# Kernel tuning notes

Hardware: AMD Instinct MI355X
Metric: run time of the kernel (lower is better)

## Reference

```python
import jax, jax.numpy as jnp
import numpy as np

D_SNP, D_MODEL, N_HEADS = 512, 512, 8
D_K = D_MODEL // N_HEADS
TEMPERATURE = 1.0
NEG = -1e9


def setup_inputs() -> dict:
    key = jax.random.key(0)
    ks = jax.random.split(key, 16)
    B, G, S = 4, 1024, 4096
    inp = {
        'queries': jax.random.normal(ks[0], (B, G, D_SNP), jnp.float32),
        'keys_values': jax.random.normal(ks[1], (B, S, D_SNP), jnp.float32),
        'dq': jax.random.normal(ks[2], (B, 1, D_MODEL), jnp.float32),
        'dk': jax.random.normal(ks[3], (B, 1, D_MODEL), jnp.float32),
        'mask': jax.random.randint(ks[4], (B, S), 0, 2, jnp.int32),
        'cis_mask': jax.random.randint(ks[5], (G, S), 0, 2, jnp.int32).astype(bool),
        'wq_w': jax.random.normal(ks[6], (D_MODEL, D_SNP), jnp.float32) * 0.02,
        'wq_b': jnp.zeros((D_MODEL,), jnp.float32),
        'wk_w': jax.random.normal(ks[7], (D_MODEL, D_SNP), jnp.float32) * 0.02,
        'wk_b': jnp.zeros((D_MODEL,), jnp.float32),
        'wv_w': jax.random.normal(ks[8], (D_MODEL, D_SNP), jnp.float32) * 0.02,
        'wv_b': jnp.zeros((D_MODEL,), jnp.float32),
        'wo_w': jax.random.normal(ks[9], (D_MODEL, D_MODEL), jnp.float32) * 0.02,
        'wo_b': jnp.zeros((D_MODEL,), jnp.float32),
        'ln_g': jnp.ones((D_MODEL,), jnp.float32),
        'ln_b': jnp.zeros((D_MODEL,), jnp.float32),
    }
    return inp


def _layer_norm(x, g, b, eps=1e-5):
    mu = jnp.mean(x, axis=-1, keepdims=True)
    var = jnp.var(x, axis=-1, keepdims=True)
    return (x - mu) * jax.lax.rsqrt(var + eps) * g + b


def reference(queries, keys_values, dq, dk, mask, cis_mask,
              wq_w, wq_b, wk_w, wk_b, wv_w, wv_b, wo_w, wo_b, ln_g, ln_b):
    B, G, _ = queries.shape
    S = keys_values.shape[1]
    # Linear projections (torch Linear: x @ W^T + b) + env shifts
    Q = queries @ wq_w.T + wq_b + dq          # [B, G, D]
    K = keys_values @ wk_w.T + wk_b + dk      # [B, S, D]
    V = keys_values @ wv_w.T + wv_b           # [B, S, D]
    # split heads: [B, H, len, d_k]
    Q = Q.reshape(B, G, N_HEADS, D_K).transpose(0, 2, 1, 3)
    K = K.reshape(B, S, N_HEADS, D_K).transpose(0, 2, 1, 3)
    V = V.reshape(B, S, N_HEADS, D_K).transpose(0, 2, 1, 3)
    scale = 1.0 / (TEMPERATURE * np.sqrt(D_K).astype(np.float32))
    scores = jnp.einsum('bhgd,bhsd->bhgs', Q, K) * scale  # [B,H,G,S]
    # cis structural mask: True = cis (kept)
    scores = jnp.where(cis_mask[None, None, :, :], scores, NEG)
    # padding mask: 1 = valid
    scores = jnp.where(mask[:, None, None, :] == 0, NEG, scores)
    attn = jax.nn.softmax(scores, axis=-1)    # dropout=0 in eval
    out = jnp.einsum('bhgs,bhsd->bhgd', attn, V)
    out = out.transpose(0, 2, 1, 3).reshape(B, G, D_MODEL)
    out = out @ wo_w.T + wo_b
    return _layer_norm(out, ln_g, ln_b)
```

## Files before the change

### kernel.cpp

```cpp
#include <hip/hip_runtime.h>
#include <stdint.h>
#include <stddef.h>

typedef __bf16 bf16;
typedef __bf16 bf16x4 __attribute__((ext_vector_type(4)));
typedef __bf16 bf16x8 __attribute__((ext_vector_type(8)));
typedef float f32x4 __attribute__((ext_vector_type(4)));
typedef float f32x16 __attribute__((ext_vector_type(16)));
typedef unsigned long long u64;

#define BATCH 4
#define G_LEN 1024
#define S_LEN 4096
#define DM 512
#define NH 8
#define DK 64
#define CIS_WORDS (G_LEN * (S_LEN / 64))
#define NQ_EL  (BATCH * G_LEN * DM)
#define NKV_EL (BATCH * S_LEN * DM)
#define NW_EL  (DM * DM)
#define PACK_BLOCKS ((CIS_WORDS + BATCH * (S_LEN / 64) + 3) / 4)
#define CVT_BLOCKS  ((NQ_EL + NKV_EL + 4 * NW_EL) / 2048)
#define QSCALE (0.125f * 1.44269504f)

__device__ __forceinline__ f32x4 mfma16(bf16x8 a, bf16x8 b, f32x4 c) {
    return __builtin_amdgcn_mfma_f32_16x16x32_bf16(a, b, c, 0, 0, 0);
}
__device__ __forceinline__ f32x16 mfma32(bf16x8 a, bf16x8 b, f32x16 c) {
    return __builtin_amdgcn_mfma_f32_32x32x16_bf16(a, b, c, 0, 0, 0);
}
__device__ __forceinline__ uint32_t cvtpk(float lo, float hi_) {
    uint32_t r;
    asm("v_cvt_pk_bf16_f32 %0, %1, %2" : "=v"(r) : "v"(lo), "v"(hi_));
    return r;
}
__device__ __forceinline__ void pswap(uint32_t& a, uint32_t& b) {
    asm("v_permlane32_swap_b32 %0, %1" : "+v"(a), "+v"(b));
}
__device__ __forceinline__ float fexp2(float x) {
    float r;
    asm("v_exp_f32 %0, %1" : "=v"(r) : "v"(x));
    return r;
}
__device__ __forceinline__ bf16x8 mk8(uint32_t a, uint32_t b, uint32_t c, uint32_t d) {
    union { uint32_t u[4]; bf16x8 v; } x;
    x.u[0] = a; x.u[1] = b; x.u[2] = c; x.u[3] = d;
    return x.v;
}
__device__ __forceinline__ void exppack(f32x16& c, uint32_t kw, float& lsum,
                                        bf16x8& pa0, bf16x8& pa1) {
    #pragma unroll
    for (int reg = 0; reg < 16; ++reg) {
        const int bit = (reg & 3) + 8 * (reg >> 2);
        const float e = fexp2(c[reg]);
        c[reg] = ((kw >> bit) & 1u) ? e : 0.f;
    }
    lsum += ((c[0] + c[1]) + (c[2] + c[3])) + ((c[4] + c[5]) + (c[6] + c[7]))
          + ((c[8] + c[9]) + (c[10] + c[11])) + ((c[12] + c[13]) + (c[14] + c[15]));
    uint32_t wa0 = cvtpk(c[0],  c[1]),  wa1 = cvtpk(c[2],  c[3]);
    uint32_t wb0 = cvtpk(c[4],  c[5]),  wb1 = cvtpk(c[6],  c[7]);
    uint32_t wc0 = cvtpk(c[8],  c[9]),  wc1 = cvtpk(c[10], c[11]);
    uint32_t wd0 = cvtpk(c[12], c[13]), wd1 = cvtpk(c[14], c[15]);
    pswap(wa0, wb0); pswap(wa1, wb1); pswap(wc0, wd0); pswap(wc1, wd1);
    pa0 = mk8(wa0, wa1, wb0, wb1);
    pa1 = mk8(wc0, wc1, wd0, wd1);
}
__device__ __forceinline__ void stage16(const bf16* g, char* l) {
    __builtin_amdgcn_global_load_lds(
        (const __attribute__((address_space(1))) void*)g,
        (__attribute__((address_space(3))) void*)l, 16, 0, 0);
}

__global__ __launch_bounds__(256) void prep(
    const void* __restrict__ cisv, const int* __restrict__ mask,
    const float* __restrict__ q, const float* __restrict__ kv,
    const float* __restrict__ wq, const float* __restrict__ wk,
    const float* __restrict__ wv, const float* __restrict__ wo,
    u64* __restrict__ cbits, u64* __restrict__ mbits,
    bf16* __restrict__ oq, bf16* __restrict__ okv, bf16* __restrict__ ow4)
{
    const int bid = blockIdx.x;
    if (bid < PACK_BLOCKS) {
        const unsigned char* cis8 = (const unsigned char*)cisv;
        const int lane = threadIdx.x & 63;
        const int is_byte = __any((int)cis8[4 * lane + 1]);
        const int wid = bid * 4 + (threadIdx.x >> 6);
        if (wid < CIS_WORDS) {
            int v;
            if (is_byte) v = cis8[(size_t)wid * 64 + lane];
            else         v = ((const int*)cisv)[(size_t)wid * 64 + lane];
            const u64 bits = __ballot(v != 0);
            if (lane == 0) cbits[wid] = bits;
        } else if (wid < CIS_WORDS + BATCH * (S_LEN / 64)) {
            const int w2 = wid - CIS_WORDS;
            const u64 bits = __ballot(mask[w2 * 64 + lane] != 0);
            if (lane == 0) mbits[w2] = bits;
        }
        return;
    }
    const size_t e = ((size_t)(bid - PACK_BLOCKS) * 256 + threadIdx.x) * 8;
    const float* src;
    bf16* dst;
    size_t off;
    if (e < NQ_EL)               { src = q;  dst = oq;  off = e; }
    else if (e < NQ_EL + NKV_EL) { src = kv; dst = okv; off = e - NQ_EL; }
    else {
        const size_t w = e - NQ_EL - NKV_EL;
        const int wi = (int)(w / NW_EL);
        off = w % NW_EL;
        src = (wi == 0) ? wq : (wi == 1) ? wk : (wi == 2) ? wv : wo;
        dst = ow4 + (size_t)wi * NW_EL;
    }
    const float4 a = *(const float4*)(src + off);
    const float4 b = *(const float4*)(src + off + 4);
    bf16x8 o;
    o[0] = (bf16)a.x; o[1] = (bf16)a.y; o[2] = (bf16)a.z; o[3] = (bf16)a.w;
    o[4] = (bf16)b.x; o[5] = (bf16)b.y; o[6] = (bf16)b.z; o[7] = (bf16)b.w;
    *(bf16x8*)(dst + off) = o;
}

template<int OUT_F32, int ROWS_PER_B>
__global__ __launch_bounds__(256) void gemm64(
    const bf16* __restrict__ A, const bf16* __restrict__ B,
    const float* __restrict__ bias, const float* __restrict__ shift,
    void* __restrict__ Out, float oscale)
{
    __shared__ bf16 As[64][72];
    __shared__ bf16 Bs[64][72];
    const int tid  = threadIdx.x;
    const int lane = tid & 63;
    const int wave = tid >> 6;
    const int l15  = lane & 15;
    const int l4   = lane >> 4;
    const int m0   = blockIdx.x * 64;
    const int n0   = blockIdx.y * 64;

    f32x4 acc[4] = {};

    for (int kt = 0; kt < DM; kt += 64) {
        #pragma unroll
        for (int i = 0; i < 2; ++i) {
            const int q   = tid + i * 256;
            const int row = q >> 3;
            const int kq  = (q & 7) * 8;
            *(bf16x8*)&As[row][kq] = *(const bf16x8*)(A + (size_t)(m0 + row) * DM + kt + kq);
            *(bf16x8*)&Bs[row][kq] = *(const bf16x8*)(B + (size_t)(n0 + row) * DM + kt + kq);
        }
        __syncthreads();
        #pragma unroll
        for (int ks = 0; ks < 64; ks += 32) {
            const bf16x8 a = *(const bf16x8*)&As[wave * 16 + l15][ks + 8 * l4];
            #pragma unroll
            for (int n = 0; n < 4; ++n) {
                const bf16x8 b = *(const bf16x8*)&Bs[n * 16 + l15][ks + 8 * l4];
                acc[n] = mfma16(a, b, acc[n]);
            }
        }
        __syncthreads();
    }

    #pragma unroll
    for (int n = 0; n < 4; ++n) {
        const int col = n0 + n * 16 + l15;
        const float bv = bias[col];
        #pragma unroll
        for (int r = 0; r < 4; ++r) {
            const int m = m0 + wave * 16 + l4 * 4 + r;
            float v = acc[n][r] + bv;
            if (shift) v += shift[(m / ROWS_PER_B) * DM + col];
            v *= oscale;
            if (OUT_F32) ((float*)Out)[(size_t)m * DM + col] = v;
            else         ((bf16*)Out)[(size_t)m * DM + col] = (bf16)v;
        }
    }
}

__global__ __launch_bounds__(256) void gemm_kvq128(
    const bf16* __restrict__ Xkv, const bf16* __restrict__ Xq,
    const bf16* __restrict__ Wk, const float* __restrict__ bk, const float* __restrict__ dkv,
    const bf16* __restrict__ Wv, const float* __restrict__ bv,
    const bf16* __restrict__ Wq, const float* __restrict__ bq, const float* __restrict__ dq,
    bf16* __restrict__ OutK, bf16* __restrict__ OutVt, bf16* __restrict__ OutQ)
{
    const int z = blockIdx.z;
    if (z == 2 && blockIdx.x >= 32) return;

    __shared__ bf16 As[128][72];
    __shared__ bf16 Bs[128][72];
    const int tid  = threadIdx.x;
    const int lane = tid & 63;
    const int wave = tid >> 6;
    const int l15  = lane & 15;
    const int l4   = lane >> 4;
    const int wr   = wave >> 1;
    const int wc   = wave & 1;
    const int m0   = blockIdx.x * 128;
    const int n0   = blockIdx.y * 128;
    const bf16* X = (z == 2) ? Xq : Xkv;
    const bf16* W = (z == 0) ? Wk : (z == 1) ? Wv : Wq;

    f32x4 acc[4][4] = {};

    for (int kt = 0; kt < DM; kt += 64) {
        #pragma unroll
        for (int i = 0; i < 4; ++i) {
            const int q   = tid + i * 256;
            const int row = q >> 3;
            const int kq  = (q & 7) * 8;
            *(bf16x8*)&As[row][kq] = *(const bf16x8*)(X + (size_t)(m0 + row) * DM + kt + kq);
            *(bf16x8*)&Bs[row][kq] = *(const bf16x8*)(W + (size_t)(n0 + row) * DM + kt + kq);
        }
        __syncthreads();
        #pragma unroll
        for (int ks = 0; ks < 64; ks += 32) {
            bf16x8 af[4];
            #pragma unroll
            for (int mi = 0; mi < 4; ++mi)
                af[mi] = *(const bf16x8*)&As[wr * 64 + mi * 16 + l15][ks + 8 * l4];
            #pragma unroll
            for (int n = 0; n < 4; ++n) {
                const bf16x8 b = *(const bf16x8*)&Bs[wc * 64 + n * 16 + l15][ks + 8 * l4];
                #pragma unroll
                for (int mi = 0; mi < 4; ++mi)
                    acc[mi][n] = mfma16(af[mi], b, acc[mi][n]);
            }
        }
        __syncthreads();
    }

    #pragma unroll
    for (int n = 0; n < 4; ++n) {
        const int col = n0 + wc * 64 + n * 16 + l15;
        #pragma unroll
        for (int mi = 0; mi < 4; ++mi) {
            const int mb = m0 + wr * 64 + mi * 16 + l4 * 4;
            if (z == 1) {
                const int bb = mb >> 12;
                const float bvc = bv[col];
                bf16x4 o;
                #pragma unroll
                for (int r = 0; r < 4; ++r) o[r] = (bf16)(acc[mi][n][r] + bvc);
                *(bf16x4*)(OutVt + ((size_t)bb * DM + col) * 4096 + (mb & 4095)) = o;
            } else if (z == 0) {
                const int bb = mb >> 12;
                const float s = bk[col] + dkv[bb * DM + col];
                #pragma unroll
                for (int r = 0; r < 4; ++r)
                    OutK[(size_t)(mb + r) * DM + col] = (bf16)(acc[mi][n][r] + s);
            } else {
                const int bb = mb >> 10;
                const float s = bq[col] + dq[bb * DM + col];
                #pragma unroll
                for (int r = 0; r < 4; ++r)
                    OutQ[(size_t)(mb + r) * DM + col] = (bf16)((acc[mi][n][r] + s) * QSCALE);
            }
        }
    }
}

__global__ __launch_bounds__(256) void attn_kernel(
    const bf16* __restrict__ Qb, const bf16* __restrict__ Kb,
    const bf16* __restrict__ Vt, const u64* __restrict__ mbits,
    const u64* __restrict__ cbits, bf16* __restrict__ PO, float* __restrict__ PL)
{
    __shared__ __align__(16) char sm[32768];

    const int tid  = threadIdx.x;
    const int lane = tid & 63;
    const int wave = tid >> 6;
    const int l31  = lane & 31;
    const int hi   = lane >> 5;

    const int flat = blockIdx.x;
    const int xcd  = flat & 7;
    const int slot = flat >> 3;
    const int pr   = xcd * 4 + (slot >> 5);
    const int sub  = slot & 31;
    const int b    = pr >> 3;
    const int h    = pr & 7;
    const int g0   = (sub >> 2) * 128;
    const int tb   = (sub & 3) * 16;
    const int blkid = pr * 32 + sub;

    const bf16* qbase = Qb + (size_t)(b * G_LEN + g0 + wave * 32 + l31) * DM + h * DK + 8 * hi;
    const bf16x8 qf0 = *(const bf16x8*)(qbase);
    const bf16x8 qf1 = *(const bf16x8*)(qbase + 16);
    const bf16x8 qf2 = *(const bf16x8*)(qbase + 32);
    const bf16x8 qf3 = *(const bf16x8*)(qbase + 48);

    const bf16* Kh = Kb + (size_t)b * S_LEN * DM + h * DK;
    const bf16* Vh = Vt + (size_t)(b * NH + h) * DK * S_LEN;
    const u64*  mbv = mbits + b * (S_LEN / 64);
    const u64*  cbv = cbits + (size_t)(g0 + wave * 32 + l31) * (S_LEN / 64);

    const bool isK    = (wave < 2);
    const int rowbase = (wave & 1) * 32 + (lane >> 3);
    const int col16s  = (lane & 7) ^ (rowbase & 7);
    const int swz     = l31 & 7;

#define STAGE(tt, bufi) do {                                                   \
    char* ldw = sm + (bufi) * 16384 + wave * 4096;                             \
    _Pragma("unroll")                                                          \
    for (int i = 0; i < 4; ++i) {                                              \
        const int row = rowbase + i * 8;                                       \
        const bf16* g = isK                                                    \
            ? (Kh + (size_t)((tt) * 64 + row) * DM + col16s * 8)               \
            : (Vh + (size_t)row * S_LEN + (tt) * 64 + col16s * 8);             \
        stage16(g, ldw + i * 1024);                                            \
    }                                                                          \
} while (0)

    f32x16 accA = {};
    f32x16 accB = {};
    float lsum = 0.f;

    STAGE(tb + 0, 0);

    for (int t = 0; t < 16; ++t) {
        __builtin_amdgcn_s_barrier();
        __builtin_amdgcn_sched_barrier(0);
        if (t + 1 < 16) {
            STAGE(tb + t + 1, (t + 1) & 1);
            asm volatile("s_waitcnt vmcnt(4)" ::: "memory");
        } else {
            asm volatile("s_waitcnt vmcnt(0)" ::: "memory");
        }
        __builtin_amdgcn_s_barrier();
        __builtin_amdgcn_sched_barrier(0);

        const char* bK = sm + (t & 1) * 16384;
        const char* bV = bK + 8192;

#define KF(ss, m) (*(const bf16x8*)(bK + ((ss) * 32 + l31) * 128 + (((2 * (m) + hi) ^ swz) * 16)))
        f32x16 c0 = {}, c1 = {};
        __builtin_amdgcn_s_setprio(1);
        c0 = mfma32(KF(0, 0), qf0, c0); c0 = mfma32(KF(0, 1), qf1, c0);
        c0 = mfma32(KF(0, 2), qf2, c0); c0 = mfma32(KF(0, 3), qf3, c0);
        c1 = mfma32(KF(1, 0), qf0, c1); c1 = mfma32(KF(1, 1), qf1, c1);
        c1 = mfma32(KF(1, 2), qf2, c1); c1 = mfma32(KF(1, 3), qf3, c1);
        __builtin_amdgcn_s_setprio(0);

        const u64 w64 = cbv[tb + t] & mbv[tb + t];
        const uint32_t kw0 = ((uint32_t)w64) >> (4 * hi);
        const uint32_t kw1 = ((uint32_t)(w64 >> 32)) >> (4 * hi);

        bf16x8 pa0, pa1, pb0, pb1;
        exppack(c0, kw0, lsum, pa0, pa1);
        exppack(c1, kw1, lsum, pb0, pb1);

#define VF(ss, ks, dh) (*(const bf16x8*)(bV + ((dh) * 32 + l31) * 128 + ((((ss) * 4 + (ks) * 2 + hi) ^ swz) * 16)))
        __builtin_amdgcn_s_setprio(1);
        accA = mfma32(pa0, VF(0, 0, 0), accA); accA = mfma32(pa1, VF(0, 1, 0), accA);
        accA = mfma32(pb0, VF(1, 0, 0), accA); accA = mfma32(pb1, VF(1, 1, 0), accA);
        accB = mfma32(pa0, VF(0, 0, 1), accB); accB = mfma32(pa1, VF(0, 1, 1), accB);
        accB = mfma32(pb0, VF(1, 0, 1), accB); accB = mfma32(pb1, VF(1, 1, 1), accB);
        __builtin_amdgcn_s_setprio(0);
    }
#undef KF
#undef VF
#undef STAGE

    const float tl = lsum + __shfl_xor(lsum, 32);
    if (hi == 0) PL[blkid * 128 + wave * 32 + l31] = tl;
    bf16* po = PO + (size_t)blkid * 8192 + (wave * 32) * 64;
    #pragma unroll
    for (int reg = 0; reg < 16; ++reg) {
        const int q = (reg & 3) + 8 * (reg >> 2) + 4 * hi;
        po[q * 64 + l31]      = (bf16)accA[reg];
        po[q * 64 + 32 + l31] = (bf16)accB[reg];
    }
}

__global__ __launch_bounds__(256) void attn_merge(
    const bf16* __restrict__ PO, const float* __restrict__ PL, bf16* __restrict__ AO)
{
    const int idx = (blockIdx.x * 256 + threadIdx.x) * 4;
    const int row = idx >> 9;
    const int col = idx & 511;
    const int h   = col >> 6;
    const int d   = col & 63;
    const int pr  = (row >> 10) * 8 + h;
    const int gt  = (row & 1023) >> 7;
    const int q   = row & 127;
    const int slot0 = pr * 32 + gt * 4;
    float num[4] = {0.f, 0.f, 0.f, 0.f};
    float pl = 0.f;
    #pragma unroll
    for (int s = 0; s < 4; ++s) {
        const bf16x4 n = *(const bf16x4*)(PO + (size_t)(slot0 + s) * 8192 + q * 64 + d);
        #pragma unroll
        for (int j = 0; j < 4; ++j) num[j] += (float)n[j];
        pl += PL[(slot0 + s) * 128 + q];
    }
    const float inv = pl > 0.f ? 1.f / pl : 0.f;
    bf16x4 o;
    #pragma unroll
    for (int j = 0; j < 4; ++j) o[j] = (bf16)(num[j] * inv);
    *(bf16x4*)(AO + (size_t)row * 512 + col) = o;
}

__global__ __launch_bounds__(256) void out_ln(
    const float* __restrict__ Y, const float* __restrict__ gam,
    const float* __restrict__ bet, float* __restrict__ out)
{
    const int row = blockIdx.x;
    const int tid = threadIdx.x;
    const float x0 = Y[(size_t)row * DM + tid];
    const float x1 = Y[(size_t)row * DM + 256 + tid];
    float s  = x0 + x1;
    float sq = x0 * x0 + x1 * x1;
    #pragma unroll
    for (int off = 1; off < 64; off <<= 1) {
        s  += __shfl_xor(s, off);
        sq += __shfl_xor(sq, off);
    }
    __shared__ float ss[4], ssq[4];
    const int wave = tid >> 6;
    if ((tid & 63) == 0) { ss[wave] = s; ssq[wave] = sq; }
    __syncthreads();
    s  = ss[0] + ss[1] + ss[2] + ss[3];
    sq = ssq[0] + ssq[1] + ssq[2] + ssq[3];
    const float mu  = s * (1.f / 512.f);
    const float var = sq * (1.f / 512.f) - mu * mu;
    const float rs  = rsqrtf(var + 1e-5f);
    out[(size_t)row * DM + tid]       = (x0 - mu) * rs * gam[tid] + bet[tid];
    out[(size_t)row * DM + 256 + tid] = (x1 - mu) * rs * gam[tid + 256] + bet[tid + 256];
}

extern "C" void kernel_launch(void* const* d_in, const int* in_sizes, int n_in,
                              void* d_out, int out_size, void* d_ws, size_t ws_size,
                              hipStream_t stream) {
    const float* queries     = (const float*)d_in[0];
    const float* keys_values = (const float*)d_in[1];
    const float* dq          = (const float*)d_in[2];
    const float* dk          = (const float*)d_in[3];
    const int*   mask        = (const int*)d_in[4];
    const void*  cis         = d_in[5];
    const float* wq_w = (const float*)d_in[6];
    const float* wq_b = (const float*)d_in[7];
    const float* wk_w = (const float*)d_in[8];
    const float* wk_b = (const float*)d_in[9];
    const float* wv_w = (const float*)d_in[10];
    const float* wv_b = (const float*)d_in[11];
    const float* wo_w = (const float*)d_in[12];
    const float* wo_b = (const float*)d_in[13];
    const float* ln_g = (const float*)d_in[14];
    const float* ln_b = (const float*)d_in[15];
    float* out = (float*)d_out;

    char* ws = (char*)d_ws;
    bf16*  Qbf = (bf16*)(ws);
    bf16*  Kbf = (bf16*)(ws + (4u << 20));
    bf16*  Vt  = (bf16*)(ws + (20u << 20));
    bf16*  AO  = (bf16*)(ws + (36u << 20));
    bf16*  Xq  = (bf16*)(ws + (36u << 20));
    bf16*  PO  = (bf16*)(ws + (40u << 20));
    bf16*  Xkv = (bf16*)(ws + (40u << 20));
    float* Yw  = (float*)(ws + (40u << 20));
    u64*   mbits   = (u64*)(ws + (56u << 20) + 4096);
    u64*   cbits   = (u64*)(ws + (56u << 20) + 8192);
    float* PL      = (float*)(ws + (56u << 20) + 544 * 1024);
    bf16*  Wb4     = (bf16*)(ws + (58u << 20));
    bf16*  Wqb = Wb4;
    bf16*  Wkb = Wb4 + (size_t)NW_EL;
    bf16*  Wvb = Wb4 + (size_t)2 * NW_EL;
    bf16*  Wob = Wb4 + (size_t)3 * NW_EL;

    prep<<<PACK_BLOCKS + CVT_BLOCKS, 256, 0, stream>>>(
        cis, mask, queries, keys_values, wq_w, wk_w, wv_w, wo_w,
        cbits, mbits, Xq, Xkv, Wb4);

    gemm_kvq128<<<dim3(128, 4, 3), 256, 0, stream>>>(
        Xkv, Xq, Wkb, wk_b, dk, Wvb, wv_b, Wqb, wq_b, dq, Kbf, Vt, Qbf);

    attn_kernel<<<1024, 256, 0, stream>>>(Qbf, Kbf, Vt, mbits, cbits, PO, PL);
    attn_merge<<<2048, 256, 0, stream>>>(PO, PL, AO);

    gemm64<1, 1024><<<dim3(64, 8), 256, 0, stream>>>(AO, Wob, wo_b, nullptr, Yw, 1.0f);

    out_ln<<<4096, 256, 0, stream>>>(Yw, ln_g, ln_b, out);
}
```

Before: 138.8 us.

## Double-buffer projection GEMM with async direct-to-LDS loads and XOR swizzle

```diff
diff --git a/kernel.cpp b/kernel.cpp
--- a/kernel.cpp
+++ b/kernel.cpp
@@ -185,8 +185,8 @@
     const int z = blockIdx.z;
     if (z == 2 && blockIdx.x >= 32) return;
 
-    __shared__ bf16 As[128][72];
-    __shared__ bf16 Bs[128][72];
+    __shared__ __align__(16) char sm[65536];
+
     const int tid  = threadIdx.x;
     const int lane = tid & 63;
     const int wave = tid >> 6;
@@ -199,34 +199,52 @@
     const bf16* X = (z == 2) ? Xq : Xkv;
     const bf16* W = (z == 0) ? Wk : (z == 1) ? Wv : Wq;
 
+    const bf16* gs  = ((wave < 2) ? X : W)
+                    + (size_t)(((wave < 2) ? m0 : n0) + (wave & 1) * 64 + (lane >> 3)) * DM
+                    + ((lane & 7) ^ (lane >> 3)) * 8;
+    const int lhalf = (wave < 2 ? 0 : 16384) + (wave & 1) * 8192;
+
+#define STAGE(kt_, bufi) do {                                                  \
+    char* ldw = sm + (bufi) * 32768 + lhalf;                                   \
+    _Pragma("unroll")                                                          \
+    for (int i = 0; i < 8; ++i)                                                \
+        stage16(gs + (kt_) * 64 + (size_t)i * 8 * DM, ldw + i * 1024);         \
+} while (0)
+
     f32x4 acc[4][4] = {};
 
-    for (int kt = 0; kt < DM; kt += 64) {
-        #pragma unroll
-        for (int i = 0; i < 4; ++i) {
-            const int q   = tid + i * 256;
-            const int row = q >> 3;
-            const int kq  = (q & 7) * 8;
-            *(bf16x8*)&As[row][kq] = *(const bf16x8*)(X + (size_t)(m0 + row) * DM + kt + kq);
-            *(bf16x8*)&Bs[row][kq] = *(const bf16x8*)(W + (size_t)(n0 + row) * DM + kt + kq);
-        }
-        __syncthreads();
+    STAGE(0, 0);
+    for (int kt = 0; kt < 8; ++kt) {
+        __builtin_amdgcn_s_barrier();
+        __builtin_amdgcn_sched_barrier(0);
+        if (kt + 1 < 8) {
+            STAGE(kt + 1, (kt + 1) & 1);
+            asm volatile("s_waitcnt vmcnt(8)" ::: "memory");
+        } else {
+            asm volatile("s_waitcnt vmcnt(0)" ::: "memory");
+        }
+        __builtin_amdgcn_s_barrier();
+        __builtin_amdgcn_sched_barrier(0);
+
+        const char* bA = sm + (kt & 1) * 32768;
+        const char* bB = bA + 16384;
         #pragma unroll
         for (int ks = 0; ks < 64; ks += 32) {
+            const int slotx = (4 * (ks >> 5) + l4) ^ (l15 & 7);
             bf16x8 af[4];
             #pragma unroll
             for (int mi = 0; mi < 4; ++mi)
-                af[mi] = *(const bf16x8*)&As[wr * 64 + mi * 16 + l15][ks + 8 * l4];
+                af[mi] = *(const bf16x8*)(bA + (wr * 64 + mi * 16 + l15) * 128 + slotx * 16);
             #pragma unroll
             for (int n = 0; n < 4; ++n) {
-                const bf16x8 b = *(const bf16x8*)&Bs[wc * 64 + n * 16 + l15][ks + 8 * l4];
+                const bf16x8 b = *(const bf16x8*)(bB + (wc * 64 + n * 16 + l15) * 128 + slotx * 16);
                 #pragma unroll
                 for (int mi = 0; mi < 4; ++mi)
                     acc[mi][n] = mfma16(af[mi], b, acc[mi][n]);
             }
         }
-        __syncthreads();
-    }
+    }
+#undef STAGE
 
     #pragma unroll
     for (int n = 0; n < 4; ++n) {
```

After: 136.8 us, median of 2. About the same (-1.4%).
